# Performance work log

Hardware: AMD Instinct MI355X
Metric: run time of the kernel (lower is better)

Reference implementation:

```python
import jax, jax.numpy as jnp
import numpy as np

T, H, E, K = 256, 2048, 60, 4          # tokens, hidden, num_experts, top_k
F, FS = 1408, 5632                      # moe_intermediate, shared_expert_intermediate


def setup_inputs() -> dict:
    key = jax.random.key(0)
    ks = jax.random.split(key, 9)
    s = 0.02  # weight init scale to keep activations sane
    return {
        "hidden_states": jax.random.normal(ks[0], (T, H), jnp.float32),
        "gate_w": jax.random.normal(ks[1], (H, E), jnp.float32) * s,       # router
        "w_gate": jax.random.normal(ks[2], (E, H, F), jnp.float32) * s,    # expert gate proj
        "w_up": jax.random.normal(ks[3], (E, H, F), jnp.float32) * s,      # expert up proj
        "w_down": jax.random.normal(ks[4], (E, F, H), jnp.float32) * s,    # expert down proj
        "sw_gate": jax.random.normal(ks[5], (H, FS), jnp.float32) * s,     # shared expert gate proj
        "sw_up": jax.random.normal(ks[6], (H, FS), jnp.float32) * s,       # shared expert up proj
        "sw_down": jax.random.normal(ks[7], (FS, H), jnp.float32) * s,     # shared expert down proj
        "shared_gate_w": jax.random.normal(ks[8], (H, 1), jnp.float32) * s,  # shared expert sigmoid gate
    }


def reference(hidden_states, gate_w, w_gate, w_up, w_down, sw_gate, sw_up, sw_down, shared_gate_w):
    x = hidden_states                                  # [T, H]
    # --- router: softmax then top-k (DefaultMoeRoutingMethod, no renorm) ---
    probs = jax.nn.softmax(x @ gate_w, axis=-1)        # [T, E]
    vals, idx = jax.lax.top_k(probs, K)                # [T, K]
    tok = jnp.arange(x.shape[0])[:, None]
    comb = jnp.zeros_like(probs).at[tok, idx].set(vals)  # dense combine weights [T, E]
    # --- experts: gated SiLU MLP per expert, combine-weighted (down is linear,
    #     so scaling the pre-down activation by comb equals scaling the output) ---
    g = jnp.einsum('th,ehf->tef', x, w_gate)           # [T, E, F]
    u = jnp.einsum('th,ehf->tef', x, w_up)             # [T, E, F]
    a = (jax.nn.silu(g) * u) * comb[:, :, None]
    moe_out = jnp.einsum('tef,efh->th', a, w_down)     # [T, H]
    # --- shared expert with sigmoid gate ---
    sh = (jax.nn.silu(x @ sw_gate) * (x @ sw_up)) @ sw_down   # [T, H]
    sh = jax.nn.sigmoid(x @ shared_gate_w) * sh
    return moe_out + sh
```

## Files before the change

kernel.cpp:

```cpp
#include <hip/hip_runtime.h>
#include <hip/hip_bf16.h>
#include <stdint.h>

typedef unsigned short ushort_t;
typedef uint32_t u32;
typedef __attribute__((ext_vector_type(8))) __bf16 bf16x8;
typedef __attribute__((ext_vector_type(8))) unsigned short u16x8;
typedef __attribute__((ext_vector_type(4))) float f32x4;

#define T_  256
#define H_  2048
#define E_  60
#define F_  1408
#define FS_ 5632

__device__ __forceinline__ u32 rne2(float lo, float hi){
  u32 a = __builtin_bit_cast(u32, lo);
  u32 b = __builtin_bit_cast(u32, hi);
  a += 0x7FFFu + ((a >> 16) & 1u);
  b += 0x7FFFu + ((b >> 16) & 1u);
  return (a >> 16) | (b & 0xFFFF0000u);
}
__device__ __forceinline__ ushort_t rne1(float f){
  u32 a = __builtin_bit_cast(u32, f);
  a += 0x7FFFu + ((a >> 16) & 1u);
  return (ushort_t)(a >> 16);
}
__device__ __forceinline__ f32x4 zero4(){ f32x4 z; z[0]=0.f; z[1]=0.f; z[2]=0.f; z[3]=0.f; return z; }

__device__ __forceinline__ bf16x8 ldsbS(const float* p, const int S){
  union { u32 u[4]; bf16x8 v; } cv;
  cv.u[0] = rne2(p[0],   p[S]);
  cv.u[1] = rne2(p[2*S], p[3*S]);
  cv.u[2] = rne2(p[4*S], p[5*S]);
  cv.u[3] = rne2(p[6*S], p[7*S]);
  return cv.v;
}
__device__ __forceinline__ bf16x8 loada(const ushort_t* p){
  return __builtin_bit_cast(bf16x8, *(const u16x8*)p);
}
__device__ __forceinline__ void gload16(const float* g, float* l){
  __builtin_amdgcn_global_load_lds(
      (const __attribute__((address_space(1))) void*)g,
      (__attribute__((address_space(3))) void*)l, 16, 0, 0);
}
#define MFMA(a,b,c) __builtin_amdgcn_mfma_f32_16x16x32_bf16((a),(b),(c),0,0,0)

#define VMW(n)  asm volatile("s_waitcnt vmcnt(" #n ")" ::: "memory")
#define BARM()  asm volatile("s_barrier" ::: "memory")
#define SCH()   __builtin_amdgcn_sched_barrier(0)

__global__ __launch_bounds__(256) void k_router(
    const float* __restrict__ x, const float* __restrict__ gw,
    const float* __restrict__ sgw, ushort_t* __restrict__ xb,
    int* __restrict__ tk_idx, float* __restrict__ tk_val, float* __restrict__ sig)
{
  const int t = blockIdx.x, tid = threadIdx.x;
  const float* xr = x + (size_t)t * H_;
  {
    const float4 v0 = *(const float4*)(xr + tid*8);
    const float4 v1 = *(const float4*)(xr + tid*8 + 4);
    u32* dst = (u32*)(xb + (size_t)t*H_ + tid*8);
    dst[0] = rne2(v0.x, v0.y); dst[1] = rne2(v0.z, v0.w);
    dst[2] = rne2(v1.x, v1.y); dst[3] = rne2(v1.z, v1.w);
  }
  __shared__ float s_part[4][64];
  __shared__ float s_logit[64];
  __shared__ float s_red[256];
  const int e = tid & 63, q = tid >> 6;
  float p = 0.f;
  if (e < E_) {
    const float* g = gw + e;
    for (int h = q*512; h < q*512 + 512; ++h) p += xr[h] * g[h*E_];
  }
  s_part[q][e] = p;
  float sp = 0.f;
  for (int h = tid; h < H_; h += 256) sp += xr[h] * sgw[h];
  s_red[tid] = sp;
  __syncthreads();
  if (tid < 64) s_logit[tid] = s_part[0][tid] + s_part[1][tid] + s_part[2][tid] + s_part[3][tid];
  for (int s = 128; s > 0; s >>= 1) {
    if (tid < s) s_red[tid] += s_red[tid + s];
    __syncthreads();
  }
  if (tid == 0) {
    sig[t] = 1.f / (1.f + expf(-s_red[0]));
    float mx = -3.4e38f;
    for (int i = 0; i < E_; ++i) mx = fmaxf(mx, s_logit[i]);
    float sum = 0.f;
    for (int i = 0; i < E_; ++i) sum += expf(s_logit[i] - mx);
    for (int k = 0; k < 4; ++k) {
      float bv = -3.4e38f; int bi = 0;
      for (int i = 0; i < E_; ++i) { float v = s_logit[i]; if (v > bv) { bv = v; bi = i; } }
      tk_idx[t*4 + k] = bi;
      tk_val[t*4 + k] = expf(bv - mx) / sum;
      s_logit[bi] = -3.4e38f;
    }
  }
}

__global__ __launch_bounds__(256) void k_lists(
    const int* __restrict__ tk_idx, const float* __restrict__ tk_val,
    int* __restrict__ cnt, int* __restrict__ ltok,
    int* __restrict__ lpair, float* __restrict__ lwt)
{
  __shared__ int   s_idx[1024];
  __shared__ float s_val[1024];
  const int tid = threadIdx.x;
  for (int i = tid; i < 1024; i += 256) { s_idx[i] = tk_idx[i]; s_val[i] = tk_val[i]; }
  __syncthreads();
  const int e = tid;
  if (e >= E_) return;
  int c = 0;
  for (int i = 0; i < 1024; ++i) {
    if (s_idx[i] == e && c < 64) {
      ltok[e*64 + c]  = i >> 2;
      lpair[e*64 + c] = i;
      lwt[e*64 + c]   = s_val[i];
      ++c;
    }
  }
  cnt[e] = c;
}

__global__ __launch_bounds__(256) void k_mega1(
    const ushort_t* __restrict__ xb,
    const float* __restrict__ wg_all, const float* __restrict__ wu_all,
    const int* __restrict__ cnt, const int* __restrict__ ltok,
    const float* __restrict__ lwt, ushort_t* __restrict__ act,
    const float* __restrict__ swg, const float* __restrict__ swu,
    ushort_t* __restrict__ acts)
{
  __shared__ char smem[65536];
  float* lds = (float*)smem;
  const int bid = blockIdx.x;
  const int tid = threadIdx.x, wave = tid >> 6, lane = tid & 63;
  const int ln15 = lane & 15, kg = lane >> 4;

  if (bid < 660) {
    const int e  = bid / 11;
    const int cx = bid % 11;
    int m = cnt[e];
    if (m == 0) return;
    if (m > 64) m = 64;
    const int col0 = cx * 128;
    const size_t wbase = (size_t)e * ((size_t)H_ * F_) + col0;
    const float* gsg = wg_all + wbase + (size_t)(lane >> 5) * F_ + (lane & 31) * 4;
    const float* gsu = wu_all + wbase + (size_t)(lane >> 5) * F_ + (lane & 31) * 4;
    const int r0 = wave * 8;

    const ushort_t* ap[4];
    #pragma unroll
    for (int rt = 0; rt < 4; ++rt) {
      int row = rt*16 + ln15;
      int tok = ltok[e*64 + (row < m ? row : m-1)];
      ap[rt] = xb + (size_t)tok * H_ + kg*8;
    }

    f32x4 ag[4][2], au[4][2];
    #pragma unroll
    for (int i = 0; i < 4; ++i) { ag[i][0]=zero4(); ag[i][1]=zero4(); au[i][0]=zero4(); au[i][1]=zero4(); }
    bf16x8 a0[4], a1[4];

#define GU_STAGE(B, K0) do { \
    _Pragma("unroll") for (int i2 = 0; i2 < 4; ++i2) { \
      int r_ = r0 + i2*2; \
      gload16(gsg + (size_t)(K0 + r_) * F_, lds + (B)*8192 + r_*128); \
      gload16(gsu + (size_t)(K0 + r_) * F_, lds + (B)*8192 + 4096 + r_*128); \
    } } while(0)
#define GU_ALOAD(D, K0) do { \
    _Pragma("unroll") for (int rt = 0; rt < 4; ++rt) D[rt] = loada(ap[rt] + (K0)); } while(0)
#define GU_COMPUTE(B, A) do { \
    const float* lg_ = lds + (B)*8192 + kg*1024 + wave*32 + ln15; \
    bf16x8 bg0_ = ldsbS(lg_, 128), bg1_ = ldsbS(lg_ + 16, 128); \
    bf16x8 bu0_ = ldsbS(lg_ + 4096, 128), bu1_ = ldsbS(lg_ + 4112, 128); \
    _Pragma("unroll") for (int rt = 0; rt < 4; ++rt) { \
      ag[rt][0] = MFMA(A[rt], bg0_, ag[rt][0]); \
      ag[rt][1] = MFMA(A[rt], bg1_, ag[rt][1]); \
      au[rt][0] = MFMA(A[rt], bu0_, au[rt][0]); \
      au[rt][1] = MFMA(A[rt], bu1_, au[rt][1]); \
    } } while(0)

    GU_ALOAD(a0, 0);  GU_STAGE(0, 0);
    GU_ALOAD(a1, 32); GU_STAGE(1, 32);
    for (int t = 0; t + 2 < 64; t += 2) {
      VMW(12); BARM(); SCH();
      GU_COMPUTE(0, a0);
      BARM();
      GU_ALOAD(a0, (t+2)*32); GU_STAGE(0, (t+2)*32);
      VMW(12); BARM(); SCH();
      GU_COMPUTE(1, a1);
      BARM();
      GU_ALOAD(a1, (t+3)*32); GU_STAGE(1, (t+3)*32);
    }
    VMW(12); BARM(); SCH();
    GU_COMPUTE(0, a0);
    VMW(0); BARM(); SCH();
    GU_COMPUTE(1, a1);

    #pragma unroll
    for (int rt = 0; rt < 4; ++rt)
      #pragma unroll
      for (int nt = 0; nt < 2; ++nt)
        #pragma unroll
        for (int j = 0; j < 4; ++j) {
          int r = rt*16 + kg*4 + j;
          if (r < m) {
            float wt = lwt[e*64 + r];
            float g = ag[rt][nt][j], u = au[rt][nt][j];
            float a = g / (1.f + __expf(-g)) * u * wt;
            act[((size_t)e*64 + r) * F_ + col0 + wave*32 + nt*16 + ln15] = rne1(a);
          }
        }
  } else {
    const int sb = bid - 660;
    const int cb = sb * 32;
    const int rowb = wave * 64;
    const int r0 = wave * 8;
    const float* gsg = swg + (size_t)(lane >> 3) * FS_ + cb + (lane & 7) * 4;
    const float* gsu = swu + (size_t)(lane >> 3) * FS_ + cb + (lane & 7) * 4;

    const ushort_t* ap[4];
    #pragma unroll
    for (int rt = 0; rt < 4; ++rt)
      ap[rt] = xb + (size_t)(rowb + rt*16 + ln15) * H_ + kg*8;

    f32x4 ag[4][2], au[4][2];
    #pragma unroll
    for (int i = 0; i < 4; ++i) { ag[i][0]=zero4(); ag[i][1]=zero4(); au[i][0]=zero4(); au[i][1]=zero4(); }
    bf16x8 a0[4], a1[4];

#define SG_STAGE(B, K0) do { \
    gload16(gsg + (size_t)(K0 + r0) * FS_, lds + (B)*2048 + r0*32); \
    gload16(gsu + (size_t)(K0 + r0) * FS_, lds + (B)*2048 + 1024 + r0*32); \
  } while(0)
#define SG_ALOAD(D, K0) do { \
    _Pragma("unroll") for (int rt = 0; rt < 4; ++rt) D[rt] = loada(ap[rt] + (K0)); } while(0)
#define SG_COMPUTE(B, A) do { \
    const float* lg_ = lds + (B)*2048 + kg*256 + ln15; \
    bf16x8 bg0_ = ldsbS(lg_, 32), bg1_ = ldsbS(lg_ + 16, 32); \
    bf16x8 bu0_ = ldsbS(lg_ + 1024, 32), bu1_ = ldsbS(lg_ + 1040, 32); \
    _Pragma("unroll") for (int rt = 0; rt < 4; ++rt) { \
      ag[rt][0] = MFMA(A[rt], bg0_, ag[rt][0]); \
      ag[rt][1] = MFMA(A[rt], bg1_, ag[rt][1]); \
      au[rt][0] = MFMA(A[rt], bu0_, au[rt][0]); \
      au[rt][1] = MFMA(A[rt], bu1_, au[rt][1]); \
    } } while(0)

    SG_ALOAD(a0, 0);  SG_STAGE(0, 0);
    SG_ALOAD(a1, 32); SG_STAGE(1, 32);
    for (int t = 0; t + 2 < 64; t += 2) {
      VMW(6); BARM(); SCH();
      SG_COMPUTE(0, a0);
      BARM();
      SG_ALOAD(a0, (t+2)*32); SG_STAGE(0, (t+2)*32);
      VMW(6); BARM(); SCH();
      SG_COMPUTE(1, a1);
      BARM();
      SG_ALOAD(a1, (t+3)*32); SG_STAGE(1, (t+3)*32);
    }
    VMW(6); BARM(); SCH();
    SG_COMPUTE(0, a0);
    VMW(0); BARM(); SCH();
    SG_COMPUTE(1, a1);

    #pragma unroll
    for (int rt = 0; rt < 4; ++rt)
      #pragma unroll
      for (int nt = 0; nt < 2; ++nt)
        #pragma unroll
        for (int j = 0; j < 4; ++j) {
          int row = rowb + rt*16 + kg*4 + j;
          float g = ag[rt][nt][j], u = au[rt][nt][j];
          acts[(size_t)row * FS_ + cb + nt*16 + ln15] = rne1(g / (1.f + __expf(-g)) * u);
        }
  }
}

__global__ __launch_bounds__(256) void k_mega2(
    const ushort_t* __restrict__ act, const float* __restrict__ wd_all,
    const int* __restrict__ cnt, const int* __restrict__ lpair,
    float* __restrict__ out4,
    const ushort_t* __restrict__ acts, const float* __restrict__ swd,
    float* __restrict__ acc4)
{
  __shared__ char smem[65536];
  float* lds = (float*)smem;
  const int bid = blockIdx.x;
  const int tid = threadIdx.x, wave = tid >> 6, lane = tid & 63;
  const int ln15 = lane & 15, kg = lane >> 4;

  if (bid < 480) {
    const int e  = bid / 8;
    const int cx = bid % 8;
    int m = cnt[e];
    if (m == 0) return;
    if (m > 64) m = 64;
    __shared__ int s_pair[64];
    if (tid < 64) s_pair[tid] = (tid < m) ? lpair[e*64 + tid] : 0;
    const int col0 = cx * 256;
    const float* gsd = wd_all + (size_t)e * ((size_t)F_ * H_) + col0 + lane * 4;
    const int r0 = wave * 8;
    const int c0 = wave * 64;

    const ushort_t* ap[4];
    #pragma unroll
    for (int rt = 0; rt < 4; ++rt)
      ap[rt] = act + ((size_t)e*64 + rt*16 + ln15) * F_ + kg*8;

    f32x4 ac[4][4];
    #pragma unroll
    for (int i = 0; i < 4; ++i)
      #pragma unroll
      for (int c = 0; c < 4; ++c) ac[i][c] = zero4();
    bf16x8 a0[4], a1[4];

#define DN_STAGE(B, K0) do { \
    _Pragma("unroll") for (int i2 = 0; i2 < 8; ++i2) { \
      int r_ = r0 + i2; \
      gload16(gsd + (size_t)(K0 + r_) * H_, lds + (B)*8192 + r_*256); \
    } } while(0)
#define DN_ALOAD(D, K0) do { \
    _Pragma("unroll") for (int rt = 0; rt < 4; ++rt) D[rt] = loada(ap[rt] + (K0)); } while(0)
#define DN_COMPUTE(B, A) do { \
    const float* lw_ = lds + (B)*8192 + kg*2048 + c0 + ln15; \
    bf16x8 b0_ = ldsbS(lw_, 256),      b1_ = ldsbS(lw_ + 16, 256); \
    bf16x8 b2_ = ldsbS(lw_ + 32, 256), b3_ = ldsbS(lw_ + 48, 256); \
    _Pragma("unroll") for (int rt = 0; rt < 4; ++rt) { \
      ac[rt][0] = MFMA(A[rt], b0_, ac[rt][0]); \
      ac[rt][1] = MFMA(A[rt], b1_, ac[rt][1]); \
      ac[rt][2] = MFMA(A[rt], b2_, ac[rt][2]); \
      ac[rt][3] = MFMA(A[rt], b3_, ac[rt][3]); \
    } } while(0)

    DN_ALOAD(a0, 0);  DN_STAGE(0, 0);
    DN_ALOAD(a1, 32); DN_STAGE(1, 32);
    for (int t = 0; t + 2 < 44; t += 2) {
      VMW(12); BARM(); SCH();
      DN_COMPUTE(0, a0);
      BARM();
      DN_ALOAD(a0, (t+2)*32); DN_STAGE(0, (t+2)*32);
      VMW(12); BARM(); SCH();
      DN_COMPUTE(1, a1);
      BARM();
      DN_ALOAD(a1, (t+3)*32); DN_STAGE(1, (t+3)*32);
    }
    VMW(12); BARM(); SCH();
    DN_COMPUTE(0, a0);
    VMW(0); BARM(); SCH();
    DN_COMPUTE(1, a1);

    #pragma unroll
    for (int rt = 0; rt < 4; ++rt)
      #pragma unroll
      for (int c = 0; c < 4; ++c)
        #pragma unroll
        for (int j = 0; j < 4; ++j) {
          int r = rt*16 + kg*4 + j;
          if (r < m)
            out4[(size_t)s_pair[r] * H_ + col0 + c0 + c*16 + ln15] = ac[rt][c][j];
        }
  } else {
    const int sb = bid - 480;
    const int cb = (sb & 31) * 64;
    const int kh = sb >> 5;
    const int rowb = wave * 64;
    const int r0 = wave * 8;
    const float* gsd = swd + (size_t)(kh*1408) * H_ + cb
                     + (size_t)(lane >> 4) * H_ + (lane & 15) * 4;

    const ushort_t* ap[4];
    #pragma unroll
    for (int rt = 0; rt < 4; ++rt)
      ap[rt] = acts + (size_t)(rowb + rt*16 + ln15) * FS_ + kh*1408 + kg*8;

    f32x4 ac[4][4];
    #pragma unroll
    for (int i = 0; i < 4; ++i)
      #pragma unroll
      for (int c = 0; c < 4; ++c) ac[i][c] = zero4();
    bf16x8 a0[4], a1[4];

#define SD_STAGE(B, K0) do { \
    gload16(gsd + (size_t)(K0 + r0) * H_,     lds + (B)*2048 + r0*64); \
    gload16(gsd + (size_t)(K0 + r0 + 4) * H_, lds + (B)*2048 + (r0+4)*64); \
  } while(0)
#define SD_ALOAD(D, K0) do { \
    _Pragma("unroll") for (int rt = 0; rt < 4; ++rt) D[rt] = loada(ap[rt] + (K0)); } while(0)
#define SD_COMPUTE(B, A) do { \
    const float* lw_ = lds + (B)*2048 + kg*512 + ln15; \
    bf16x8 b0_ = ldsbS(lw_, 64),      b1_ = ldsbS(lw_ + 16, 64); \
    bf16x8 b2_ = ldsbS(lw_ + 32, 64), b3_ = ldsbS(lw_ + 48, 64); \
    _Pragma("unroll") for (int rt = 0; rt < 4; ++rt) { \
      ac[rt][0] = MFMA(A[rt], b0_, ac[rt][0]); \
      ac[rt][1] = MFMA(A[rt], b1_, ac[rt][1]); \
      ac[rt][2] = MFMA(A[rt], b2_, ac[rt][2]); \
      ac[rt][3] = MFMA(A[rt], b3_, ac[rt][3]); \
    } } while(0)

    SD_ALOAD(a0, 0);  SD_STAGE(0, 0);
    SD_ALOAD(a1, 32); SD_STAGE(1, 32);
    for (int t = 0; t + 2 < 44; t += 2) {
      VMW(6); BARM(); SCH();
      SD_COMPUTE(0, a0);
      BARM();
      SD_ALOAD(a0, (t+2)*32); SD_STAGE(0, (t+2)*32);
      VMW(6); BARM(); SCH();
      SD_COMPUTE(1, a1);
      BARM();
      SD_ALOAD(a1, (t+3)*32); SD_STAGE(1, (t+3)*32);
    }
    VMW(6); BARM(); SCH();
    SD_COMPUTE(0, a0);
    VMW(0); BARM(); SCH();
    SD_COMPUTE(1, a1);

    #pragma unroll
    for (int rt = 0; rt < 4; ++rt)
      #pragma unroll
      for (int c = 0; c < 4; ++c)
        #pragma unroll
        for (int j = 0; j < 4; ++j) {
          int row = rowb + rt*16 + kg*4 + j;
          acc4[((size_t)kh * T_ + row) * H_ + cb + c*16 + ln15] = ac[rt][c][j];
        }
  }
}

__global__ __launch_bounds__(256) void k_final(
    const float* __restrict__ acc4, const float* __restrict__ out4,
    const float* __restrict__ sig, float* __restrict__ out)
{
  const int idx = blockIdx.x * blockDim.x + threadIdx.x;
  const int t = idx >> 9;
  const int h = (idx & 511) * 4;
  float ox = 0.f, oy = 0.f, oz = 0.f, ow = 0.f;
  #pragma unroll
  for (int s = 0; s < 4; ++s) {
    const float4 v = *(const float4*)(acc4 + ((size_t)s * T_ + t) * H_ + h);
    ox += v.x; oy += v.y; oz += v.z; ow += v.w;
  }
  const float sg = sig[t];
  ox *= sg; oy *= sg; oz *= sg; ow *= sg;
  #pragma unroll
  for (int k = 0; k < 4; ++k) {
    const float4 e4 = *(const float4*)(out4 + (size_t)(t*4 + k) * H_ + h);
    ox += e4.x; oy += e4.y; oz += e4.z; ow += e4.w;
  }
  float4 o; o.x = ox; o.y = oy; o.z = oz; o.w = ow;
  *(float4*)(out + (size_t)t * H_ + h) = o;
}

extern "C" void kernel_launch(void* const* d_in, const int* in_sizes, int n_in,
                              void* d_out, int out_size, void* d_ws, size_t ws_size,
                              hipStream_t stream)
{
  (void)in_sizes; (void)n_in; (void)out_size; (void)ws_size;
  const float* x   = (const float*)d_in[0];
  const float* gw  = (const float*)d_in[1];
  const float* wg  = (const float*)d_in[2];
  const float* wu  = (const float*)d_in[3];
  const float* wd  = (const float*)d_in[4];
  const float* swg = (const float*)d_in[5];
  const float* swu = (const float*)d_in[6];
  const float* swd = (const float*)d_in[7];
  const float* sgw = (const float*)d_in[8];

  char* ws = (char*)d_ws;
  ushort_t* xb    = (ushort_t*)(ws);
  ushort_t* act   = (ushort_t*)(ws + 1048576);
  ushort_t* acts  = (ushort_t*)(ws + 11862016);
  float*    out4  = (float*)   (ws + 14745600);
  float*    acc4  = (float*)   (ws + 23134208);
  float*    sig   = (float*)   (ws + 31522816);
  int*      tkidx = (int*)     (ws + 31523840);
  float*    tkval = (float*)   (ws + 31527936);
  int*      cnt   = (int*)     (ws + 31532032);
  int*      ltok  = (int*)     (ws + 31532288);
  int*      lpair = (int*)     (ws + 31547648);
  float*    lwt   = (float*)   (ws + 31563008);

  k_router<<<T_, 256, 0, stream>>>(x, gw, sgw, xb, tkidx, tkval, sig);
  k_lists <<<1, 256, 0, stream>>>(tkidx, tkval, cnt, ltok, lpair, lwt);
  k_mega1 <<<660 + 176, 256, 0, stream>>>(xb, wg, wu, cnt, ltok, lwt, act, swg, swu, acts);
  k_mega2 <<<480 + 128, 256, 0, stream>>>(act, wd, cnt, lpair, out4, acts, swd, acc4);
  k_final <<<512, 256, 0, stream>>>(acc4, out4, sig, (float*)d_out);
}
```

Measured before the change: 615.8 us.

## Widen MoE GEMM tiles to 512-thread blocks with larger LDS staging

Both mega kernels move from 256 to 512 threads per block and use wider column tiles: 176 columns per expert block in gate/up, 512 in down, and doubled tiles for the shared expert. The global-to-LDS staging is rewritten as byte-offset chunked loads, so each block stages a wider weight slab in one pass. The aim is fewer blocks, less redundant activation loading per weight byte, and more waves available to hide latency. In exchange it uses 92-128KB of LDS per block, which limits occupancy, and the 176-column split leaves uneven work across waves (waves 3-7 carry one n-tile instead of two).

Measured after the change: 690.1 us. 12.1% more time.

```diff
diff --git a/kernel.cpp b/kernel.cpp
--- a/kernel.cpp
+++ b/kernel.cpp
@@ -123,7 +123,7 @@
   cnt[e] = c;
 }
 
-__global__ __launch_bounds__(256) void k_mega1(
+__global__ __launch_bounds__(512) void k_mega1(
     const ushort_t* __restrict__ xb,
     const float* __restrict__ wg_all, const float* __restrict__ wu_all,
     const int* __restrict__ cnt, const int* __restrict__ ltok,
@@ -131,23 +131,26 @@
     const float* __restrict__ swg, const float* __restrict__ swu,
     ushort_t* __restrict__ acts)
 {
-  __shared__ char smem[65536];
+  __shared__ char smem[94208];
   float* lds = (float*)smem;
   const int bid = blockIdx.x;
   const int tid = threadIdx.x, wave = tid >> 6, lane = tid & 63;
   const int ln15 = lane & 15, kg = lane >> 4;
 
-  if (bid < 660) {
-    const int e  = bid / 11;
-    const int cx = bid % 11;
+  if (bid < 480) {
+    const int e  = bid >> 3;
+    const int cx = bid & 7;
     int m = cnt[e];
     if (m == 0) return;
     if (m > 64) m = 64;
-    const int col0 = cx * 128;
+    const int col0 = cx * 176;
     const size_t wbase = (size_t)e * ((size_t)H_ * F_) + col0;
-    const float* gsg = wg_all + wbase + (size_t)(lane >> 5) * F_ + (lane & 31) * 4;
-    const float* gsu = wu_all + wbase + (size_t)(lane >> 5) * F_ + (lane & 31) * 4;
-    const int r0 = wave * 8;
+    const char* gsg = (const char*)(wg_all + wbase);
+    const char* gsu = (const char*)(wu_all + wbase);
+    const int nreal = (wave < 4) ? 6 : 5;
+    const int sbeg  = (wave < 4) ? 6*wave : 24 + 5*(wave - 4);
+    const int has2  = (wave < 3);
+    const int n0c = wave*16, n1c = (wave+8)*16;
 
     const ushort_t* ap[4];
     #pragma unroll
@@ -162,46 +165,63 @@
     for (int i = 0; i < 4; ++i) { ag[i][0]=zero4(); ag[i][1]=zero4(); au[i][0]=zero4(); au[i][1]=zero4(); }
     bf16x8 a0[4], a1[4];
 
-#define GU_STAGE(B, K0) do { \
-    _Pragma("unroll") for (int i2 = 0; i2 < 4; ++i2) { \
-      int r_ = r0 + i2*2; \
-      gload16(gsg + (size_t)(K0 + r_) * F_, lds + (B)*8192 + r_*128); \
-      gload16(gsu + (size_t)(K0 + r_) * F_, lds + (B)*8192 + 4096 + r_*128); \
-    } } while(0)
-#define GU_ALOAD(D, K0) do { \
+#define GU2_STAGE(B, K0) do { \
+    _Pragma("unroll") for (int n_ = 0; n_ < 6; ++n_) { \
+      if (n_ < nreal) { \
+        int i_ = sbeg + n_; \
+        int off_ = i_*1024 + (lane<<4); \
+        int mo_ = (i_ < 22) ? off_ : off_ - 22528; \
+        int row_ = mo_ / 704; \
+        int colb_ = mo_ - row_*704; \
+        const char* s_ = ((i_ < 22) ? gsg : gsu) + (size_t)((K0) + row_)*(F_*4) + colb_; \
+        gload16((const float*)s_, (float*)(smem + (B)*45056 + i_*1024)); \
+      } else { \
+        const char* s_ = gsg + (size_t)(K0)*(F_*4) + (lane<<4); \
+        gload16((const float*)s_, (float*)(smem + 90112 + (wave-4)*1024)); \
+      } \
+    } } while(0)
+#define GU2_ALOAD(D, K0) do { \
     _Pragma("unroll") for (int rt = 0; rt < 4; ++rt) D[rt] = loada(ap[rt] + (K0)); } while(0)
-#define GU_COMPUTE(B, A) do { \
-    const float* lg_ = lds + (B)*8192 + kg*1024 + wave*32 + ln15; \
-    bf16x8 bg0_ = ldsbS(lg_, 128), bg1_ = ldsbS(lg_ + 16, 128); \
-    bf16x8 bu0_ = ldsbS(lg_ + 4096, 128), bu1_ = ldsbS(lg_ + 4112, 128); \
+#define GU2_COMPUTE(B, A) do { \
+    const float* bb_ = lds + (B)*11264 + kg*8*176; \
+    bf16x8 bg0_ = ldsbS(bb_ + n0c + ln15, 176); \
+    bf16x8 bu0_ = ldsbS(bb_ + 5632 + n0c + ln15, 176); \
     _Pragma("unroll") for (int rt = 0; rt < 4; ++rt) { \
       ag[rt][0] = MFMA(A[rt], bg0_, ag[rt][0]); \
-      ag[rt][1] = MFMA(A[rt], bg1_, ag[rt][1]); \
       au[rt][0] = MFMA(A[rt], bu0_, au[rt][0]); \
-      au[rt][1] = MFMA(A[rt], bu1_, au[rt][1]); \
-    } } while(0)
-
-    GU_ALOAD(a0, 0);  GU_STAGE(0, 0);
-    GU_ALOAD(a1, 32); GU_STAGE(1, 32);
+    } \
+    if (has2) { \
+      bf16x8 bg1_ = ldsbS(bb_ + n1c + ln15, 176); \
+      bf16x8 bu1_ = ldsbS(bb_ + 5632 + n1c + ln15, 176); \
+      _Pragma("unroll") for (int rt = 0; rt < 4; ++rt) { \
+        ag[rt][1] = MFMA(A[rt], bg1_, ag[rt][1]); \
+        au[rt][1] = MFMA(A[rt], bu1_, au[rt][1]); \
+      } \
+    } } while(0)
+
+    GU2_ALOAD(a0, 0);  GU2_STAGE(0, 0);
+    GU2_ALOAD(a1, 32); GU2_STAGE(1, 32);
     for (int t = 0; t + 2 < 64; t += 2) {
-      VMW(12); BARM(); SCH();
-      GU_COMPUTE(0, a0);
-      BARM();
-      GU_ALOAD(a0, (t+2)*32); GU_STAGE(0, (t+2)*32);
-      VMW(12); BARM(); SCH();
-      GU_COMPUTE(1, a1);
-      BARM();
-      GU_ALOAD(a1, (t+3)*32); GU_STAGE(1, (t+3)*32);
-    }
-    VMW(12); BARM(); SCH();
-    GU_COMPUTE(0, a0);
+      VMW(10); BARM(); SCH();
+      GU2_COMPUTE(0, a0);
+      BARM();
+      GU2_ALOAD(a0, (t+2)*32); GU2_STAGE(0, (t+2)*32);
+      VMW(10); BARM(); SCH();
+      GU2_COMPUTE(1, a1);
+      BARM();
+      GU2_ALOAD(a1, (t+3)*32); GU2_STAGE(1, (t+3)*32);
+    }
+    VMW(10); BARM(); SCH();
+    GU2_COMPUTE(0, a0);
     VMW(0); BARM(); SCH();
-    GU_COMPUTE(1, a1);
-
-    #pragma unroll
-    for (int rt = 0; rt < 4; ++rt)
+    GU2_COMPUTE(1, a1);
+
+    #pragma unroll
+    for (int nt = 0; nt < 2; ++nt) {
+      if (nt == 1 && !has2) break;
+      int coln = col0 + (nt ? n1c : n0c) + ln15;
       #pragma unroll
-      for (int nt = 0; nt < 2; ++nt)
+      for (int rt = 0; rt < 4; ++rt)
         #pragma unroll
         for (int j = 0; j < 4; ++j) {
           int r = rt*16 + kg*4 + j;
@@ -209,16 +229,17 @@
             float wt = lwt[e*64 + r];
             float g = ag[rt][nt][j], u = au[rt][nt][j];
             float a = g / (1.f + __expf(-g)) * u * wt;
-            act[((size_t)e*64 + r) * F_ + col0 + wave*32 + nt*16 + ln15] = rne1(a);
+            act[((size_t)e*64 + r) * F_ + coln] = rne1(a);
           }
         }
+    }
   } else {
-    const int sb = bid - 660;
-    const int cb = sb * 32;
-    const int rowb = wave * 64;
-    const int r0 = wave * 8;
-    const float* gsg = swg + (size_t)(lane >> 3) * FS_ + cb + (lane & 7) * 4;
-    const float* gsu = swu + (size_t)(lane >> 3) * FS_ + cb + (lane & 7) * 4;
+    const int sb = bid - 480;
+    const int cb = sb * 64;
+    const int wq = wave & 3, wc = wave >> 2;
+    const int rowb = wq * 64;
+    const char* gG = (const char*)(swg + cb);
+    const char* gU = (const char*)(swu + cb);
 
     const ushort_t* ap[4];
     #pragma unroll
@@ -230,16 +251,20 @@
     for (int i = 0; i < 4; ++i) { ag[i][0]=zero4(); ag[i][1]=zero4(); au[i][0]=zero4(); au[i][1]=zero4(); }
     bf16x8 a0[4], a1[4];
 
-#define SG_STAGE(B, K0) do { \
-    gload16(gsg + (size_t)(K0 + r0) * FS_, lds + (B)*2048 + r0*32); \
-    gload16(gsu + (size_t)(K0 + r0) * FS_, lds + (B)*2048 + 1024 + r0*32); \
-  } while(0)
-#define SG_ALOAD(D, K0) do { \
+#define SG2_STAGE(B, K0) do { \
+    _Pragma("unroll") for (int n_ = 0; n_ < 2; ++n_) { \
+      int i_ = 2*wave + n_; \
+      int row_ = 4*(i_ & 7) + (lane >> 4); \
+      int colb_ = (lane & 15) << 4; \
+      const char* s_ = ((i_ < 8) ? gG : gU) + (size_t)((K0) + row_)*(FS_*4) + colb_; \
+      gload16((const float*)s_, (float*)(smem + (B)*16384 + i_*1024)); \
+    } } while(0)
+#define SG2_ALOAD(D, K0) do { \
     _Pragma("unroll") for (int rt = 0; rt < 4; ++rt) D[rt] = loada(ap[rt] + (K0)); } while(0)
-#define SG_COMPUTE(B, A) do { \
-    const float* lg_ = lds + (B)*2048 + kg*256 + ln15; \
-    bf16x8 bg0_ = ldsbS(lg_, 32), bg1_ = ldsbS(lg_ + 16, 32); \
-    bf16x8 bu0_ = ldsbS(lg_ + 1024, 32), bu1_ = ldsbS(lg_ + 1040, 32); \
+#define SG2_COMPUTE(B, A) do { \
+    const float* bb_ = lds + (B)*4096 + kg*8*64 + wc*32; \
+    bf16x8 bg0_ = ldsbS(bb_ + ln15, 64),        bg1_ = ldsbS(bb_ + 16 + ln15, 64); \
+    bf16x8 bu0_ = ldsbS(bb_ + 2048 + ln15, 64), bu1_ = ldsbS(bb_ + 2064 + ln15, 64); \
     _Pragma("unroll") for (int rt = 0; rt < 4; ++rt) { \
       ag[rt][0] = MFMA(A[rt], bg0_, ag[rt][0]); \
       ag[rt][1] = MFMA(A[rt], bg1_, ag[rt][1]); \
@@ -247,22 +272,22 @@
       au[rt][1] = MFMA(A[rt], bu1_, au[rt][1]); \
     } } while(0)
 
-    SG_ALOAD(a0, 0);  SG_STAGE(0, 0);
-    SG_ALOAD(a1, 32); SG_STAGE(1, 32);
+    SG2_ALOAD(a0, 0);  SG2_STAGE(0, 0);
+    SG2_ALOAD(a1, 32); SG2_STAGE(1, 32);
     for (int t = 0; t + 2 < 64; t += 2) {
       VMW(6); BARM(); SCH();
-      SG_COMPUTE(0, a0);
-      BARM();
-      SG_ALOAD(a0, (t+2)*32); SG_STAGE(0, (t+2)*32);
+      SG2_COMPUTE(0, a0);
+      BARM();
+      SG2_ALOAD(a0, (t+2)*32); SG2_STAGE(0, (t+2)*32);
       VMW(6); BARM(); SCH();
-      SG_COMPUTE(1, a1);
-      BARM();
-      SG_ALOAD(a1, (t+3)*32); SG_STAGE(1, (t+3)*32);
+      SG2_COMPUTE(1, a1);
+      BARM();
+      SG2_ALOAD(a1, (t+3)*32); SG2_STAGE(1, (t+3)*32);
     }
     VMW(6); BARM(); SCH();
-    SG_COMPUTE(0, a0);
+    SG2_COMPUTE(0, a0);
     VMW(0); BARM(); SCH();
-    SG_COMPUTE(1, a1);
+    SG2_COMPUTE(1, a1);
 
     #pragma unroll
     for (int rt = 0; rt < 4; ++rt)
@@ -272,35 +297,34 @@
         for (int j = 0; j < 4; ++j) {
           int row = rowb + rt*16 + kg*4 + j;
           float g = ag[rt][nt][j], u = au[rt][nt][j];
-          acts[(size_t)row * FS_ + cb + nt*16 + ln15] = rne1(g / (1.f + __expf(-g)) * u);
+          acts[(size_t)row * FS_ + cb + wc*32 + nt*16 + ln15] = rne1(g / (1.f + __expf(-g)) * u);
         }
   }
 }
 
-__global__ __launch_bounds__(256) void k_mega2(
+__global__ __launch_bounds__(512) void k_mega2(
     const ushort_t* __restrict__ act, const float* __restrict__ wd_all,
     const int* __restrict__ cnt, const int* __restrict__ lpair,
     float* __restrict__ out4,
     const ushort_t* __restrict__ acts, const float* __restrict__ swd,
     float* __restrict__ acc4)
 {
-  __shared__ char smem[65536];
+  __shared__ char smem[131072];
+  __shared__ int s_pair[64];
   float* lds = (float*)smem;
   const int bid = blockIdx.x;
   const int tid = threadIdx.x, wave = tid >> 6, lane = tid & 63;
   const int ln15 = lane & 15, kg = lane >> 4;
 
-  if (bid < 480) {
-    const int e  = bid / 8;
-    const int cx = bid % 8;
+  if (bid < 240) {
+    const int e  = bid >> 2;
+    const int cx = bid & 3;
     int m = cnt[e];
     if (m == 0) return;
     if (m > 64) m = 64;
-    __shared__ int s_pair[64];
     if (tid < 64) s_pair[tid] = (tid < m) ? lpair[e*64 + tid] : 0;
-    const int col0 = cx * 256;
-    const float* gsd = wd_all + (size_t)e * ((size_t)F_ * H_) + col0 + lane * 4;
-    const int r0 = wave * 8;
+    const int col0 = cx * 512;
+    const char* gsd = (const char*)(wd_all + (size_t)e * ((size_t)F_ * H_) + col0);
     const int c0 = wave * 64;
 
     const ushort_t* ap[4];
@@ -315,17 +339,18 @@
       for (int c = 0; c < 4; ++c) ac[i][c] = zero4();
     bf16x8 a0[4], a1[4];
 
-#define DN_STAGE(B, K0) do { \
-    _Pragma("unroll") for (int i2 = 0; i2 < 8; ++i2) { \
-      int r_ = r0 + i2; \
-      gload16(gsd + (size_t)(K0 + r_) * H_, lds + (B)*8192 + r_*256); \
-    } } while(0)
-#define DN_ALOAD(D, K0) do { \
+#define DN2_STAGE(B, K0) do { \
+    _Pragma("unroll") for (int n_ = 0; n_ < 8; ++n_) { \
+      int i_ = wave + n_*8; \
+      const char* s_ = gsd + (size_t)((K0) + (i_ >> 1))*(H_*4) + (i_ & 1)*1024 + (lane << 4); \
+      gload16((const float*)s_, (float*)(smem + (B)*65536 + i_*1024)); \
+    } } while(0)
+#define DN2_ALOAD(D, K0) do { \
     _Pragma("unroll") for (int rt = 0; rt < 4; ++rt) D[rt] = loada(ap[rt] + (K0)); } while(0)
-#define DN_COMPUTE(B, A) do { \
-    const float* lw_ = lds + (B)*8192 + kg*2048 + c0 + ln15; \
-    bf16x8 b0_ = ldsbS(lw_, 256),      b1_ = ldsbS(lw_ + 16, 256); \
-    bf16x8 b2_ = ldsbS(lw_ + 32, 256), b3_ = ldsbS(lw_ + 48, 256); \
+#define DN2_COMPUTE(B, A) do { \
+    const float* bb_ = lds + (B)*16384 + kg*8*512 + c0; \
+    bf16x8 b0_ = ldsbS(bb_ + ln15, 512),      b1_ = ldsbS(bb_ + 16 + ln15, 512); \
+    bf16x8 b2_ = ldsbS(bb_ + 32 + ln15, 512), b3_ = ldsbS(bb_ + 48 + ln15, 512); \
     _Pragma("unroll") for (int rt = 0; rt < 4; ++rt) { \
       ac[rt][0] = MFMA(A[rt], b0_, ac[rt][0]); \
       ac[rt][1] = MFMA(A[rt], b1_, ac[rt][1]); \
@@ -333,22 +358,22 @@
       ac[rt][3] = MFMA(A[rt], b3_, ac[rt][3]); \
     } } while(0)
 
-    DN_ALOAD(a0, 0);  DN_STAGE(0, 0);
-    DN_ALOAD(a1, 32); DN_STAGE(1, 32);
+    DN2_ALOAD(a0, 0);  DN2_STAGE(0, 0);
+    DN2_ALOAD(a1, 32); DN2_STAGE(1, 32);
     for (int t = 0; t + 2 < 44; t += 2) {
       VMW(12); BARM(); SCH();
-      DN_COMPUTE(0, a0);
-      BARM();
-      DN_ALOAD(a0, (t+2)*32); DN_STAGE(0, (t+2)*32);
+      DN2_COMPUTE(0, a0);
+      BARM();
+      DN2_ALOAD(a0, (t+2)*32); DN2_STAGE(0, (t+2)*32);
       VMW(12); BARM(); SCH();
-      DN_COMPUTE(1, a1);
-      BARM();
-      DN_ALOAD(a1, (t+3)*32); DN_STAGE(1, (t+3)*32);
+      DN2_COMPUTE(1, a1);
+      BARM();
+      DN2_ALOAD(a1, (t+3)*32); DN2_STAGE(1, (t+3)*32);
     }
     VMW(12); BARM(); SCH();
-    DN_COMPUTE(0, a0);
+    DN2_COMPUTE(0, a0);
     VMW(0); BARM(); SCH();
-    DN_COMPUTE(1, a1);
+    DN2_COMPUTE(1, a1);
 
     #pragma unroll
     for (int rt = 0; rt < 4; ++rt)
@@ -361,13 +386,12 @@
             out4[(size_t)s_pair[r] * H_ + col0 + c0 + c*16 + ln15] = ac[rt][c][j];
         }
   } else {
-    const int sb = bid - 480;
-    const int cb = (sb & 31) * 64;
-    const int kh = sb >> 5;
-    const int rowb = wave * 64;
-    const int r0 = wave * 8;
-    const float* gsd = swd + (size_t)(kh*1408) * H_ + cb
-                     + (size_t)(lane >> 4) * H_ + (lane & 15) * 4;
+    const int sb = bid - 240;
+    const int cb = (sb & 15) * 128;
+    const int kh = sb >> 4;
+    const int wq = wave & 3, wc = wave >> 2;
+    const int rowb = wq * 64;
+    const char* gsd = (const char*)(swd + (size_t)(kh*1408) * H_ + cb);
 
     const ushort_t* ap[4];
     #pragma unroll
@@ -381,16 +405,18 @@
       for (int c = 0; c < 4; ++c) ac[i][c] = zero4();
     bf16x8 a0[4], a1[4];
 
-#define SD_STAGE(B, K0) do { \
-    gload16(gsd + (size_t)(K0 + r0) * H_,     lds + (B)*2048 + r0*64); \
-    gload16(gsd + (size_t)(K0 + r0 + 4) * H_, lds + (B)*2048 + (r0+4)*64); \
-  } while(0)
-#define SD_ALOAD(D, K0) do { \
+#define SD2_STAGE(B, K0) do { \
+    _Pragma("unroll") for (int n_ = 0; n_ < 2; ++n_) { \
+      int i_ = 2*wave + n_; \
+      const char* s_ = gsd + (size_t)((K0) + 2*i_ + (lane >> 5))*(H_*4) + ((lane & 31) << 4); \
+      gload16((const float*)s_, (float*)(smem + (B)*16384 + i_*1024)); \
+    } } while(0)
+#define SD2_ALOAD(D, K0) do { \
     _Pragma("unroll") for (int rt = 0; rt < 4; ++rt) D[rt] = loada(ap[rt] + (K0)); } while(0)
-#define SD_COMPUTE(B, A) do { \
-    const float* lw_ = lds + (B)*2048 + kg*512 + ln15; \
-    bf16x8 b0_ = ldsbS(lw_, 64),      b1_ = ldsbS(lw_ + 16, 64); \
-    bf16x8 b2_ = ldsbS(lw_ + 32, 64), b3_ = ldsbS(lw_ + 48, 64); \
+#define SD2_COMPUTE(B, A) do { \
+    const float* bb_ = lds + (B)*4096 + kg*8*128 + wc*64; \
+    bf16x8 b0_ = ldsbS(bb_ + ln15, 128),      b1_ = ldsbS(bb_ + 16 + ln15, 128); \
+    bf16x8 b2_ = ldsbS(bb_ + 32 + ln15, 128), b3_ = ldsbS(bb_ + 48 + ln15, 128); \
     _Pragma("unroll") for (int rt = 0; rt < 4; ++rt) { \
       ac[rt][0] = MFMA(A[rt], b0_, ac[rt][0]); \
       ac[rt][1] = MFMA(A[rt], b1_, ac[rt][1]); \
@@ -398,22 +424,22 @@
       ac[rt][3] = MFMA(A[rt], b3_, ac[rt][3]); \
     } } while(0)
 
-    SD_ALOAD(a0, 0);  SD_STAGE(0, 0);
-    SD_ALOAD(a1, 32); SD_STAGE(1, 32);
+    SD2_ALOAD(a0, 0);  SD2_STAGE(0, 0);
+    SD2_ALOAD(a1, 32); SD2_STAGE(1, 32);
     for (int t = 0; t + 2 < 44; t += 2) {
       VMW(6); BARM(); SCH();
-      SD_COMPUTE(0, a0);
-      BARM();
-      SD_ALOAD(a0, (t+2)*32); SD_STAGE(0, (t+2)*32);
+      SD2_COMPUTE(0, a0);
+      BARM();
+      SD2_ALOAD(a0, (t+2)*32); SD2_STAGE(0, (t+2)*32);
       VMW(6); BARM(); SCH();
-      SD_COMPUTE(1, a1);
-      BARM();
-      SD_ALOAD(a1, (t+3)*32); SD_STAGE(1, (t+3)*32);
+      SD2_COMPUTE(1, a1);
+      BARM();
+      SD2_ALOAD(a1, (t+3)*32); SD2_STAGE(1, (t+3)*32);
     }
     VMW(6); BARM(); SCH();
-    SD_COMPUTE(0, a0);
+    SD2_COMPUTE(0, a0);
     VMW(0); BARM(); SCH();
-    SD_COMPUTE(1, a1);
+    SD2_COMPUTE(1, a1);
 
     #pragma unroll
     for (int rt = 0; rt < 4; ++rt)
@@ -422,7 +448,7 @@
         #pragma unroll
         for (int j = 0; j < 4; ++j) {
           int row = rowb + rt*16 + kg*4 + j;
-          acc4[((size_t)kh * T_ + row) * H_ + cb + c*16 + ln15] = ac[rt][c][j];
+          acc4[((size_t)kh * T_ + row) * H_ + cb + wc*64 + c*16 + ln15] = ac[rt][c][j];
         }
   }
 }
@@ -482,7 +508,7 @@
 
   k_router<<<T_, 256, 0, stream>>>(x, gw, sgw, xb, tkidx, tkval, sig);
   k_lists <<<1, 256, 0, stream>>>(tkidx, tkval, cnt, ltok, lpair, lwt);
-  k_mega1 <<<660 + 176, 256, 0, stream>>>(xb, wg, wu, cnt, ltok, lwt, act, swg, swu, acts);
-  k_mega2 <<<480 + 128, 256, 0, stream>>>(act, wd, cnt, lpair, out4, acts, swd, acc4);
+  k_mega1 <<<480 + 88, 512, 0, stream>>>(xb, wg, wu, cnt, ltok, lwt, act, swg, swu, acts);
+  k_mega2 <<<240 + 64, 512, 0, stream>>>(act, wd, cnt, lpair, out4, acts, swd, acc4);
   k_final <<<512, 256, 0, stream>>>(acc4, out4, sig, (float*)d_out);
 }
```
